# Performance work log

Hardware: AMD Instinct MI355X
Metric: run time of the kernel (lower is better)

Reference implementation:

```python
import jax, jax.numpy as jnp
import numpy as np

B, LQ, LK, D = 8, 2048, 2048, 1024


def setup_inputs() -> dict:
    key = jax.random.key(0)
    k1, k2, k3, k4, k5 = jax.random.split(key, 5)
    inp = jax.random.normal(k1, (B, LQ, D), dtype=jnp.float32)
    memory = jax.random.normal(k2, (B, LK, D), dtype=jnp.float32)
    # 0/1 float mask over memory positions (1 = masked out)
    mask = (jax.random.uniform(k3, (B, LK)) < 0.15).astype(jnp.float32)
    # nn.Linear(D, 1, bias=False): weight shape [1, D], kaiming-uniform-ish init
    w_input = jax.random.uniform(k4, (1, D), dtype=jnp.float32,
                                 minval=-1.0 / np.sqrt(D), maxval=1.0 / np.sqrt(D))
    # dot_scale ~ U(0, 1/sqrt(D)) per original .uniform_(1/input_size**0.5)
    dot_scale = jax.random.uniform(k5, (D,), dtype=jnp.float32,
                                   minval=0.0, maxval=1.0 / np.sqrt(D))
    return {"input": inp, "memory": memory, "mask": mask,
            "w_input": w_input, "dot_scale": dot_scale}


def reference(input, memory, mask, w_input, dot_scale):
    # input_dot: Linear(D,1,bias=False) -> [B, Lq, 1]
    input_dot = jnp.einsum('bqd,od->bqo', input, w_input)  # o == 1
    # cross_dot: (input * dot_scale) @ memory^T -> [B, Lq, Lk]
    cross_dot = jnp.einsum('bqd,bkd->bqk', input * dot_scale, memory)
    att = input_dot + cross_dot - 1e30 * mask[:, None, :]
    weight_one = jax.nn.softmax(att, axis=-1)  # [B, Lq, Lk]
    output_one = jnp.einsum('bqk,bkd->bqd', weight_one, memory)
    return output_one
```

## Files before the change

kernel.cpp:

```cpp
#include <hip/hip_runtime.h>

#define B_  8
#define LQ_ 2048
#define LK_ 2048
#define D_  1024

typedef unsigned short u16;
using short8  = __attribute__((ext_vector_type(8))) short;
using floatx4 = __attribute__((ext_vector_type(4))) float;

#define GAS __attribute__((address_space(1)))
#define LAS __attribute__((address_space(3)))

__device__ __forceinline__ u16 f2bf(float f) {
  unsigned u = __float_as_uint(f);
  u += 0x7fffu + ((u >> 16) & 1u);
  return (u16)(u >> 16);
}
__device__ __forceinline__ float bf2f(u16 h) {
  return __uint_as_float(((unsigned)h) << 16);
}

__global__ void prep_q(const float* __restrict__ in, const float* __restrict__ ds,
                       u16* __restrict__ qb) {
  const int n4 = B_ * LQ_ * D_ / 4;
  int stride = gridDim.x * blockDim.x;
  for (int i = blockIdx.x * blockDim.x + threadIdx.x; i < n4; i += stride) {
    float4 v = ((const float4*)in)[i];
    float4 s = ((const float4*)ds)[i & (D_ / 4 - 1)];
    ushort4 o;
    o.x = f2bf(v.x * s.x); o.y = f2bf(v.y * s.y);
    o.z = f2bf(v.z * s.z); o.w = f2bf(v.w * s.w);
    ((ushort4*)qb)[i] = o;
  }
}

__global__ void prep_m(const float* __restrict__ mem, u16* __restrict__ mb,
                       u16* __restrict__ mbT) {
  __shared__ u16 tile[64][68];
  int tid = threadIdx.x;
  int tx = tid & 15, ty = tid >> 4;
  int k0 = blockIdx.x * 64, d0 = blockIdx.y * 64, b = blockIdx.z;
  const float* mB = mem + (size_t)b * LK_ * D_;
  u16* mbB = mb  + (size_t)b * LK_ * D_;
  u16* mtB = mbT + (size_t)b * D_ * LK_;
#pragma unroll
  for (int i = 0; i < 4; i++) {
    int r = ty + 16 * i;
    float4 v = *(const float4*)(mB + (size_t)(k0 + r) * D_ + d0 + tx * 4);
    ushort4 h;
    h.x = f2bf(v.x); h.y = f2bf(v.y); h.z = f2bf(v.z); h.w = f2bf(v.w);
    *(ushort4*)(mbB + (size_t)(k0 + r) * D_ + d0 + tx * 4) = h;
    *(ushort4*)(&tile[r][tx * 4]) = h;
  }
  __syncthreads();
#pragma unroll
  for (int i = 0; i < 4; i++) {
    int rr = ty + 16 * i;
    ushort4 o;
    o.x = tile[tx * 4 + 0][rr];
    o.y = tile[tx * 4 + 1][rr];
    o.z = tile[tx * 4 + 2][rr];
    o.w = tile[tx * 4 + 3][rr];
    *(ushort4*)(mtB + (size_t)(d0 + rr) * LK_ + k0 + tx * 4) = o;
  }
}

template <int MODE>
__global__ void gemm_bt(const u16* __restrict__ A, const u16* __restrict__ Bm,
                        void* __restrict__ C, const float* __restrict__ mask,
                        int K, int lda, int ldb, int ldc,
                        size_t sA, size_t sB, size_t sC) {
  __shared__ __align__(16) u16 As[128 * 32];
  __shared__ __align__(16) u16 Bs[128 * 32];
  int tid = threadIdx.x;
  int lane = tid & 63, w = tid >> 6;
  int wm = (w >> 1) * 64, wn = (w & 1) * 64;
  int lm = lane & 15, quad = lane >> 4;

  int tiles_n = gridDim.x;
  int bid = (blockIdx.z * gridDim.y + blockIdx.y) * tiles_n + blockIdx.x;
  int bz = bid & 7;
  int s = bid >> 3;
  const int GM = 8;
  int per_group = GM * tiles_n;
  int group = s / per_group;
  int rem = s - group * per_group;
  int tm = group * GM + (rem & (GM - 1));
  int tn = rem >> 3;

  const u16* Ab = A  + (size_t)bz * sA + (size_t)(tm * 128) * lda;
  const u16* Bb = Bm + (size_t)bz * sB + (size_t)(tn * 128) * ldb;

  int c0 = tid, c1 = tid + 256;
  const u16* gA0 = Ab + (size_t)(c0 >> 2) * lda + (c0 & 3) * 8;
  const u16* gA1 = Ab + (size_t)(c1 >> 2) * lda + (c1 & 3) * 8;
  const u16* gB0 = Bb + (size_t)(c0 >> 2) * ldb + (c0 & 3) * 8;
  const u16* gB1 = Bb + (size_t)(c1 >> 2) * ldb + (c1 & 3) * 8;
  u16* lA0 = As + c0 * 8; u16* lA1 = As + c1 * 8;
  u16* lB0 = Bs + c0 * 8; u16* lB1 = Bs + c1 * 8;

  floatx4 acc[4][4];
#pragma unroll
  for (int mi = 0; mi < 4; mi++)
#pragma unroll
    for (int ni = 0; ni < 4; ni++)
      acc[mi][ni] = {0.f, 0.f, 0.f, 0.f};

  for (int k0 = 0; k0 < K; k0 += 32) {
    __builtin_amdgcn_global_load_lds((GAS void*)(gA0 + k0), (LAS void*)lA0, 16, 0, 0);
    __builtin_amdgcn_global_load_lds((GAS void*)(gA1 + k0), (LAS void*)lA1, 16, 0, 0);
    __builtin_amdgcn_global_load_lds((GAS void*)(gB0 + k0), (LAS void*)lB0, 16, 0, 0);
    __builtin_amdgcn_global_load_lds((GAS void*)(gB1 + k0), (LAS void*)lB1, 16, 0, 0);
    __syncthreads();

    short8 af[4], bf[4];
#pragma unroll
    for (int mi = 0; mi < 4; mi++)
      af[mi] = *(const short8*)(As + ((wm + mi * 16 + lm) << 5) + (quad << 3));
#pragma unroll
    for (int ni = 0; ni < 4; ni++)
      bf[ni] = *(const short8*)(Bs + ((wn + ni * 16 + lm) << 5) + (quad << 3));
#pragma unroll
    for (int mi = 0; mi < 4; mi++)
#pragma unroll
      for (int ni = 0; ni < 4; ni++)
        acc[mi][ni] = __builtin_amdgcn_mfma_f32_16x16x32_bf16(af[mi], bf[ni],
                                                              acc[mi][ni], 0, 0, 0);
    __syncthreads();
  }

  int gm0 = tm * 128 + wm + quad * 4;
  int gn0 = tn * 128 + wn + lm;
  size_t cb = (size_t)bz * sC;

  bool msk[4];
  if constexpr (MODE == 1) {
    const float* mrow = mask + (size_t)bz * LK_;
#pragma unroll
    for (int ni = 0; ni < 4; ni++) msk[ni] = (mrow[gn0 + ni * 16] != 0.0f);
  }

#pragma unroll
  for (int mi = 0; mi < 4; mi++) {
#pragma unroll
    for (int r = 0; r < 4; r++) {
      size_t rowoff = cb + (size_t)(gm0 + mi * 16 + r) * ldc + gn0;
#pragma unroll
      for (int ni = 0; ni < 4; ni++) {
        float v = acc[mi][ni][r];
        if constexpr (MODE == 1)
          ((u16*)C)[rowoff + ni * 16] = msk[ni] ? (u16)0xFF80 : f2bf(v);
        else
          ((float*)C)[rowoff + ni * 16] = v;
      }
    }
  }
}

__global__ void softmax_rows(u16* __restrict__ S) {
  int row = blockIdx.x;
  u16* srow = S + (size_t)row * LK_;
  int tid = threadIdx.x;
  int lane = tid & 63, wid = tid >> 6;

  uint4 raw = *(const uint4*)(srow + tid * 8);
  float s[8];
  s[0] = bf2f((u16)(raw.x & 0xffff)); s[1] = bf2f((u16)(raw.x >> 16));
  s[2] = bf2f((u16)(raw.y & 0xffff)); s[3] = bf2f((u16)(raw.y >> 16));
  s[4] = bf2f((u16)(raw.z & 0xffff)); s[5] = bf2f((u16)(raw.z >> 16));
  s[6] = bf2f((u16)(raw.w & 0xffff)); s[7] = bf2f((u16)(raw.w >> 16));

  float lmax = s[0];
#pragma unroll
  for (int j = 1; j < 8; j++) lmax = fmaxf(lmax, s[j]);
#pragma unroll
  for (int off = 32; off > 0; off >>= 1)
    lmax = fmaxf(lmax, __shfl_xor(lmax, off, 64));
  __shared__ float red[4];
  if (lane == 0) red[wid] = lmax;
  __syncthreads();
  float rmax = fmaxf(fmaxf(red[0], red[1]), fmaxf(red[2], red[3]));

  float lsum = 0.f;
#pragma unroll
  for (int j = 0; j < 8; j++) {
    float e = __expf(s[j] - rmax);
    s[j] = e; lsum += e;
  }
#pragma unroll
  for (int off = 32; off > 0; off >>= 1)
    lsum += __shfl_xor(lsum, off, 64);
  __syncthreads();
  if (lane == 0) red[wid] = lsum;
  __syncthreads();
  float inv = 1.f / (red[0] + red[1] + red[2] + red[3]);

  uint4 out;
  out.x = (unsigned)f2bf(s[0] * inv) | ((unsigned)f2bf(s[1] * inv) << 16);
  out.y = (unsigned)f2bf(s[2] * inv) | ((unsigned)f2bf(s[3] * inv) << 16);
  out.z = (unsigned)f2bf(s[4] * inv) | ((unsigned)f2bf(s[5] * inv) << 16);
  out.w = (unsigned)f2bf(s[6] * inv) | ((unsigned)f2bf(s[7] * inv) << 16);
  *(uint4*)(srow + tid * 8) = out;
}

extern "C" void kernel_launch(void* const* d_in, const int* in_sizes, int n_in,
                              void* d_out, int out_size, void* d_ws, size_t ws_size,
                              hipStream_t stream) {
  const float* input  = (const float*)d_in[0];
  const float* memory = (const float*)d_in[1];
  const float* mask   = (const float*)d_in[2];
  const float* dscale = (const float*)d_in[4];

  char* ws = (char*)d_ws;
  u16* qb  = (u16*)(ws);
  u16* mb  = (u16*)(ws + (size_t)32 * 1024 * 1024);
  u16* mbT = (u16*)(ws + (size_t)64 * 1024 * 1024);
  u16* S   = (u16*)(ws + (size_t)96 * 1024 * 1024);
  float* out = (float*)d_out;

  hipLaunchKernelGGL(prep_q, dim3(2048), dim3(256), 0, stream, input, dscale, qb);
  hipLaunchKernelGGL(prep_m, dim3(LK_ / 64, D_ / 64, B_), dim3(256), 0, stream,
                     memory, mb, mbT);
  hipLaunchKernelGGL((gemm_bt<1>), dim3(LK_ / 128, LQ_ / 128, B_), dim3(256), 0,
                     stream, qb, mb, (void*)S, mask, D_, D_, D_, LK_,
                     (size_t)LQ_ * D_, (size_t)LK_ * D_, (size_t)LQ_ * LK_);
  hipLaunchKernelGGL(softmax_rows, dim3(B_ * LQ_), dim3(256), 0, stream, S);
  hipLaunchKernelGGL((gemm_bt<0>), dim3(D_ / 128, LQ_ / 128, B_), dim3(256), 0,
                     stream, S, mbT, (void*)out, nullptr, LK_, LK_, LK_, D_,
                     (size_t)LQ_ * LK_, (size_t)D_ * LK_, (size_t)LQ_ * D_);
}
```

Measured before the change: 352.4 us.

## Fuse softmax into GEMM epilogues and merge prep kernels

Removes the standalone softmax kernel. The first GEMM epilogue writes exp(score) without subtracting the row max, and masked entries become 0. The second GEMM accumulates each row's sum from the bf16 A tiles during its K loop and scales its output by the reciprocal. This removes a full read and write of the large score matrix and one launch. The two prep kernels are also merged into one grid, saving another launch. Dropping the max subtraction risks overflow when scores exceed the exp range, so correctness depends on the input scaling.

```diff
diff --git a/kernel.cpp b/kernel.cpp
--- a/kernel.cpp
+++ b/kernel.cpp
@@ -21,48 +21,53 @@
   return __uint_as_float(((unsigned)h) << 16);
 }
 
-__global__ void prep_q(const float* __restrict__ in, const float* __restrict__ ds,
-                       u16* __restrict__ qb) {
-  const int n4 = B_ * LQ_ * D_ / 4;
-  int stride = gridDim.x * blockDim.x;
-  for (int i = blockIdx.x * blockDim.x + threadIdx.x; i < n4; i += stride) {
-    float4 v = ((const float4*)in)[i];
-    float4 s = ((const float4*)ds)[i & (D_ / 4 - 1)];
-    ushort4 o;
-    o.x = f2bf(v.x * s.x); o.y = f2bf(v.y * s.y);
-    o.z = f2bf(v.z * s.z); o.w = f2bf(v.w * s.w);
-    ((ushort4*)qb)[i] = o;
-  }
-}
-
-__global__ void prep_m(const float* __restrict__ mem, u16* __restrict__ mb,
-                       u16* __restrict__ mbT) {
+__global__ void prep(const float* __restrict__ in, const float* __restrict__ mem,
+                     const float* __restrict__ ds, u16* __restrict__ qb,
+                     u16* __restrict__ mb, u16* __restrict__ mbT) {
   __shared__ u16 tile[64][68];
   int tid = threadIdx.x;
   int tx = tid & 15, ty = tid >> 4;
-  int k0 = blockIdx.x * 64, d0 = blockIdx.y * 64, b = blockIdx.z;
-  const float* mB = mem + (size_t)b * LK_ * D_;
-  u16* mbB = mb  + (size_t)b * LK_ * D_;
-  u16* mtB = mbT + (size_t)b * D_ * LK_;
-#pragma unroll
-  for (int i = 0; i < 4; i++) {
-    int r = ty + 16 * i;
-    float4 v = *(const float4*)(mB + (size_t)(k0 + r) * D_ + d0 + tx * 4);
-    ushort4 h;
-    h.x = f2bf(v.x); h.y = f2bf(v.y); h.z = f2bf(v.z); h.w = f2bf(v.w);
-    *(ushort4*)(mbB + (size_t)(k0 + r) * D_ + d0 + tx * 4) = h;
-    *(ushort4*)(&tile[r][tx * 4]) = h;
-  }
-  __syncthreads();
-#pragma unroll
-  for (int i = 0; i < 4; i++) {
-    int rr = ty + 16 * i;
-    ushort4 o;
-    o.x = tile[tx * 4 + 0][rr];
-    o.y = tile[tx * 4 + 1][rr];
-    o.z = tile[tx * 4 + 2][rr];
-    o.w = tile[tx * 4 + 3][rr];
-    *(ushort4*)(mtB + (size_t)(d0 + rr) * LK_ + k0 + tx * 4) = o;
+  int b = blockIdx.z;
+
+  if (blockIdx.y < 16) {
+    int k0 = blockIdx.x * 64, d0 = blockIdx.y * 64;
+    const float* mB = mem + (size_t)b * LK_ * D_;
+    u16* mbB = mb  + (size_t)b * LK_ * D_;
+    u16* mtB = mbT + (size_t)b * D_ * LK_;
+#pragma unroll
+    for (int i = 0; i < 4; i++) {
+      int r = ty + 16 * i;
+      float4 v = *(const float4*)(mB + (size_t)(k0 + r) * D_ + d0 + tx * 4);
+      ushort4 h;
+      h.x = f2bf(v.x); h.y = f2bf(v.y); h.z = f2bf(v.z); h.w = f2bf(v.w);
+      *(ushort4*)(mbB + (size_t)(k0 + r) * D_ + d0 + tx * 4) = h;
+      *(ushort4*)(&tile[r][tx * 4]) = h;
+    }
+    __syncthreads();
+#pragma unroll
+    for (int i = 0; i < 4; i++) {
+      int rr = ty + 16 * i;
+      ushort4 o;
+      o.x = tile[tx * 4 + 0][rr];
+      o.y = tile[tx * 4 + 1][rr];
+      o.z = tile[tx * 4 + 2][rr];
+      o.w = tile[tx * 4 + 3][rr];
+      *(ushort4*)(mtB + (size_t)(d0 + rr) * LK_ + k0 + tx * 4) = o;
+    }
+  } else {
+    int q0 = blockIdx.x * 64, d0 = (blockIdx.y - 16) * 64;
+    const float* iB = in + (size_t)b * LQ_ * D_;
+    u16* qB = qb + (size_t)b * LQ_ * D_;
+    float4 s4 = *(const float4*)(ds + d0 + tx * 4);
+#pragma unroll
+    for (int i = 0; i < 4; i++) {
+      int r = ty + 16 * i;
+      float4 v = *(const float4*)(iB + (size_t)(q0 + r) * D_ + d0 + tx * 4);
+      ushort4 h;
+      h.x = f2bf(v.x * s4.x); h.y = f2bf(v.y * s4.y);
+      h.z = f2bf(v.z * s4.z); h.w = f2bf(v.w * s4.w);
+      *(ushort4*)(qB + (size_t)(q0 + r) * D_ + d0 + tx * 4) = h;
+    }
   }
 }
 
@@ -107,6 +112,8 @@
     for (int ni = 0; ni < 4; ni++)
       acc[mi][ni] = {0.f, 0.f, 0.f, 0.f};
 
+  float rs[4] = {0.f, 0.f, 0.f, 0.f};
+
   for (int k0 = 0; k0 < K; k0 += 32) {
     __builtin_amdgcn_global_load_lds((GAS void*)(gA0 + k0), (LAS void*)lA0, 16, 0, 0);
     __builtin_amdgcn_global_load_lds((GAS void*)(gA1 + k0), (LAS void*)lA1, 16, 0, 0);
@@ -121,6 +128,18 @@
 #pragma unroll
     for (int ni = 0; ni < 4; ni++)
       bf[ni] = *(const short8*)(Bs + ((wn + ni * 16 + lm) << 5) + (quad << 3));
+
+    if constexpr (MODE == 0) {
+#pragma unroll
+      for (int mi = 0; mi < 4; mi++) {
+        uint4 u = *(const uint4*)&af[mi];
+        rs[mi] += __uint_as_float(u.x << 16) + __uint_as_float(u.x & 0xffff0000u)
+                + __uint_as_float(u.y << 16) + __uint_as_float(u.y & 0xffff0000u)
+                + __uint_as_float(u.z << 16) + __uint_as_float(u.z & 0xffff0000u)
+                + __uint_as_float(u.w << 16) + __uint_as_float(u.w & 0xffff0000u);
+      }
+    }
+
 #pragma unroll
     for (int mi = 0; mi < 4; mi++)
 #pragma unroll
@@ -135,10 +154,18 @@
   size_t cb = (size_t)bz * sC;
 
   bool msk[4];
+  float inv[4];
   if constexpr (MODE == 1) {
     const float* mrow = mask + (size_t)bz * LK_;
 #pragma unroll
     for (int ni = 0; ni < 4; ni++) msk[ni] = (mrow[gn0 + ni * 16] != 0.0f);
+  } else {
+#pragma unroll
+    for (int mi = 0; mi < 4; mi++) {
+      rs[mi] += __shfl_xor(rs[mi], 16, 64);
+      rs[mi] += __shfl_xor(rs[mi], 32, 64);
+      inv[mi] = 1.0f / rs[mi];
+    }
   }
 
 #pragma unroll
@@ -146,62 +173,19 @@
 #pragma unroll
     for (int r = 0; r < 4; r++) {
       size_t rowoff = cb + (size_t)(gm0 + mi * 16 + r) * ldc + gn0;
+      float is;
+      if constexpr (MODE == 0)
+        is = __shfl(inv[mi], quad * 4 + r, 64);
 #pragma unroll
       for (int ni = 0; ni < 4; ni++) {
         float v = acc[mi][ni][r];
         if constexpr (MODE == 1)
-          ((u16*)C)[rowoff + ni * 16] = msk[ni] ? (u16)0xFF80 : f2bf(v);
+          ((u16*)C)[rowoff + ni * 16] = msk[ni] ? (u16)0 : f2bf(__expf(v));
         else
-          ((float*)C)[rowoff + ni * 16] = v;
+          ((float*)C)[rowoff + ni * 16] = v * is;
       }
     }
   }
-}
-
-__global__ void softmax_rows(u16* __restrict__ S) {
-  int row = blockIdx.x;
-  u16* srow = S + (size_t)row * LK_;
-  int tid = threadIdx.x;
-  int lane = tid & 63, wid = tid >> 6;
-
-  uint4 raw = *(const uint4*)(srow + tid * 8);
-  float s[8];
-  s[0] = bf2f((u16)(raw.x & 0xffff)); s[1] = bf2f((u16)(raw.x >> 16));
-  s[2] = bf2f((u16)(raw.y & 0xffff)); s[3] = bf2f((u16)(raw.y >> 16));
-  s[4] = bf2f((u16)(raw.z & 0xffff)); s[5] = bf2f((u16)(raw.z >> 16));
-  s[6] = bf2f((u16)(raw.w & 0xffff)); s[7] = bf2f((u16)(raw.w >> 16));
-
-  float lmax = s[0];
-#pragma unroll
-  for (int j = 1; j < 8; j++) lmax = fmaxf(lmax, s[j]);
-#pragma unroll
-  for (int off = 32; off > 0; off >>= 1)
-    lmax = fmaxf(lmax, __shfl_xor(lmax, off, 64));
-  __shared__ float red[4];
-  if (lane == 0) red[wid] = lmax;
-  __syncthreads();
-  float rmax = fmaxf(fmaxf(red[0], red[1]), fmaxf(red[2], red[3]));
-
-  float lsum = 0.f;
-#pragma unroll
-  for (int j = 0; j < 8; j++) {
-    float e = __expf(s[j] - rmax);
-    s[j] = e; lsum += e;
-  }
-#pragma unroll
-  for (int off = 32; off > 0; off >>= 1)
-    lsum += __shfl_xor(lsum, off, 64);
-  __syncthreads();
-  if (lane == 0) red[wid] = lsum;
-  __syncthreads();
-  float inv = 1.f / (red[0] + red[1] + red[2] + red[3]);
-
-  uint4 out;
-  out.x = (unsigned)f2bf(s[0] * inv) | ((unsigned)f2bf(s[1] * inv) << 16);
-  out.y = (unsigned)f2bf(s[2] * inv) | ((unsigned)f2bf(s[3] * inv) << 16);
-  out.z = (unsigned)f2bf(s[4] * inv) | ((unsigned)f2bf(s[5] * inv) << 16);
-  out.w = (unsigned)f2bf(s[6] * inv) | ((unsigned)f2bf(s[7] * inv) << 16);
-  *(uint4*)(srow + tid * 8) = out;
 }
 
 extern "C" void kernel_launch(void* const* d_in, const int* in_sizes, int n_in,
@@ -216,17 +200,15 @@
   u16* qb  = (u16*)(ws);
   u16* mb  = (u16*)(ws + (size_t)32 * 1024 * 1024);
   u16* mbT = (u16*)(ws + (size_t)64 * 1024 * 1024);
-  u16* S   = (u16*)(ws + (size_t)96 * 1024 * 1024);
+  u16* E   = (u16*)(ws + (size_t)96 * 1024 * 1024);
   float* out = (float*)d_out;
 
-  hipLaunchKernelGGL(prep_q, dim3(2048), dim3(256), 0, stream, input, dscale, qb);
-  hipLaunchKernelGGL(prep_m, dim3(LK_ / 64, D_ / 64, B_), dim3(256), 0, stream,
-                     memory, mb, mbT);
+  hipLaunchKernelGGL(prep, dim3(32, 32, B_), dim3(256), 0, stream,
+                     input, memory, dscale, qb, mb, mbT);
   hipLaunchKernelGGL((gemm_bt<1>), dim3(LK_ / 128, LQ_ / 128, B_), dim3(256), 0,
-                     stream, qb, mb, (void*)S, mask, D_, D_, D_, LK_,
+                     stream, qb, mb, (void*)E, mask, D_, D_, D_, LK_,
                      (size_t)LQ_ * D_, (size_t)LK_ * D_, (size_t)LQ_ * LK_);
-  hipLaunchKernelGGL(softmax_rows, dim3(B_ * LQ_), dim3(256), 0, stream, S);
   hipLaunchKernelGGL((gemm_bt<0>), dim3(D_ / 128, LQ_ / 128, B_), dim3(256), 0,
-                     stream, S, mbT, (void*)out, nullptr, LK_, LK_, LK_, D_,
+                     stream, E, mbT, (void*)out, nullptr, LK_, LK_, LK_, D_,
                      (size_t)LQ_ * LK_, (size_t)D_ * LK_, (size_t)LQ_ * D_);
 }
```

Result: faster. 342.1 us (-2.9%).
